# Kernel optimization log

Hardware: AMD Instinct MI355X
Metric: run time of the kernel (lower is better)

## Reference

```python
import jax, jax.numpy as jnp
import numpy as np

NUM_BLOCK = 8
CHANNELS = 256
SCALE = 0.02


def setup_inputs() -> dict:
    key = jax.random.key(0)
    k1, k2, k3, k4, k5, k6 = jax.random.split(key, 6)
    real = jax.random.normal(k1, (4, 4096, NUM_BLOCK, CHANNELS), dtype=jnp.float32)
    imag = jax.random.normal(k2, (4, 4096, NUM_BLOCK, CHANNELS), dtype=jnp.float32)
    w_r = jax.random.normal(k3, (NUM_BLOCK, CHANNELS, CHANNELS), dtype=jnp.float32) * SCALE
    w_i = jax.random.normal(k4, (NUM_BLOCK, CHANNELS, CHANNELS), dtype=jnp.float32) * SCALE
    b_r = jax.random.normal(k5, (NUM_BLOCK, CHANNELS), dtype=jnp.float32) * SCALE
    b_i = jax.random.normal(k6, (NUM_BLOCK, CHANNELS), dtype=jnp.float32) * SCALE
    return {"real": real, "imag": imag, "w_r": w_r, "w_i": w_i, "b_r": b_r, "b_i": b_i}


def _mm(x, w):
    # x: [..., b, d], w: [b, d, k] -> [..., b, k]
    return jnp.einsum('...bd,bdk->...bk', x, w)


def reference(real, imag, w_r, w_i, b_r, b_i):
    out_r = _mm(real, w_r) - _mm(imag, w_i) + b_r
    out_i = _mm(real, w_i) + _mm(imag, w_r) + b_i
    return (out_r, out_i)
```

## Files before the change

kernel.cpp:

```cpp
#include <hip/hip_runtime.h>
#include <hip/hip_bf16.h>

#define NB 8
#define CH 256
#define MTOT 16384
#define ROWSTRIDE 2048
#define BM 128
#define KSTEPS 8
#define LDSPITCH 40
#define ABUF 10240
#define AIOFF 5120
#define OFFI 33554432l

typedef __attribute__((ext_vector_type(8))) short bf16x8;
typedef __attribute__((ext_vector_type(4))) float f32x4;

__device__ inline short f2bf(float f) {
    union { float f; unsigned u; } x{f};
    unsigned r = x.u + 0x7fff + ((x.u >> 16) & 1);
    return (short)(r >> 16);
}

__global__ void prep_w(const float* __restrict__ wr, const float* __restrict__ wi,
                       unsigned short* __restrict__ wT) {
    int blk = blockIdx.x;
    int mat = blk >> 8;
    int idx = blk & 255;
    int nc = idx & 3, kc = (idx >> 2) & 7, b = idx >> 5;
    const float* w = mat ? wi : wr;
    __shared__ float tile[32][65];
    int t = threadIdx.x;
    int dd = t >> 3;
    int nn = (t & 7) * 8;
    const float* src = w + (((size_t)b * 256 + kc * 32 + dd) * 256 + nc * 64 + nn);
#pragma unroll
    for (int j = 0; j < 8; ++j) tile[dd][nn + j] = src[j];
    __syncthreads();
    int n = t >> 2;
    int ds = (t & 3) * 8;
    bf16x8 p;
#pragma unroll
    for (int j = 0; j < 8; ++j) p[j] = f2bf(tile[ds + j][n]);
    unsigned short* dst = wT + (size_t)mat * 524288 + b * 65536 + kc * 8192
                             + (nc * 64 + n) * 32 + ds;
    *(bf16x8*)dst = p;
}

__launch_bounds__(512, 2)
__global__ void cgemm(const float* __restrict__ Ar, const float* __restrict__ Ai,
                      const unsigned short* __restrict__ wT,
                      const float* __restrict__ br, const float* __restrict__ bi,
                      float* __restrict__ out) {
    int bid = blockIdx.x;
    int b  = bid & 7;
    int mt = bid >> 3;

    __shared__ unsigned short lds[2 * ABUF];

    int t = threadIdx.x;
    int lane = t & 63;
    int wv = t >> 6;
    int wr_ = wv >> 2;
    int wc_ = wv & 3;
    int lrow = lane & 15;
    int kseg = lane >> 4;

    int srow = t >> 2;
    int sseg = t & 3;
    const size_t a_base = (size_t)(mt * BM + srow) * ROWSTRIDE + b * CH + sseg * 8;

    const unsigned short* wbase = wT + (size_t)b * 65536
                                     + (wc_ * 64 + lrow) * 32 + kseg * 8;

    f32x4 accr[4][4] = {};
    f32x4 acci[4][4] = {};

    f32x4 rR0, rR1, rI0, rI1;
    bf16x8 rwr[2][4], rwi[2][4];

#define LOADA(K) { const float* p = Ar + a_base + (size_t)(K) * 32;              \
                   rR0 = *(const f32x4*)p;  rR1 = *(const f32x4*)(p + 4);        \
                   const float* q = Ai + a_base + (size_t)(K) * 32;              \
                   rI0 = *(const f32x4*)q;  rI1 = *(const f32x4*)(q + 4); }
#define LOADW(SEL, K) {                                                          \
    const unsigned short* p = wbase + (size_t)(K) * 8192;                        \
    rwr[SEL][0] = *(const bf16x8*)p;                                             \
    rwr[SEL][1] = *(const bf16x8*)(p + 512);                                     \
    rwr[SEL][2] = *(const bf16x8*)(p + 1024);                                    \
    rwr[SEL][3] = *(const bf16x8*)(p + 1536);                                    \
    rwi[SEL][0] = *(const bf16x8*)(p + 524288);                                  \
    rwi[SEL][1] = *(const bf16x8*)(p + 524800);                                  \
    rwi[SEL][2] = *(const bf16x8*)(p + 525312);                                  \
    rwi[SEL][3] = *(const bf16x8*)(p + 525824); }
#define STAGEA(BUF) {                                                            \
    bf16x8 pr, pi;                                                               \
    _Pragma("unroll")                                                            \
    for (int j = 0; j < 4; ++j) { pr[j] = f2bf(rR0[j]); pr[j + 4] = f2bf(rR1[j]);\
                                  pi[j] = f2bf(rI0[j]); pi[j + 4] = f2bf(rI1[j]);}\
    int d0 = (BUF) * ABUF + srow * LDSPITCH + sseg * 8;                          \
    *(bf16x8*)&lds[d0]         = pr;                                             \
    *(bf16x8*)&lds[d0 + AIOFF] = pi; }

    LOADA(0);
    LOADW(0, 0);
    STAGEA(0);

#pragma unroll
    for (int kk = 0; kk < KSTEPS; ++kk) {
        __syncthreads();
        if (kk + 1 < KSTEPS) {
            LOADA(kk + 1);
            LOADW((kk + 1) & 1, kk + 1);
        }
        int ab = (kk & 1) * ABUF;
#pragma unroll
        for (int mf = 0; mf < 4; ++mf) {
            int off = ab + (wr_ * 64 + mf * 16 + lrow) * LDSPITCH + kseg * 8;
            bf16x8 ar = *(const bf16x8*)&lds[off];
            bf16x8 ai = *(const bf16x8*)&lds[off + AIOFF];
            bf16x8 ain = ai ^ (short)0x8000;
#pragma unroll
            for (int nf = 0; nf < 4; ++nf) {
                accr[mf][nf] = __builtin_amdgcn_mfma_f32_16x16x32_bf16(ar,  rwr[kk & 1][nf], accr[mf][nf], 0, 0, 0);
                accr[mf][nf] = __builtin_amdgcn_mfma_f32_16x16x32_bf16(ain, rwi[kk & 1][nf], accr[mf][nf], 0, 0, 0);
                acci[mf][nf] = __builtin_amdgcn_mfma_f32_16x16x32_bf16(ar,  rwi[kk & 1][nf], acci[mf][nf], 0, 0, 0);
                acci[mf][nf] = __builtin_amdgcn_mfma_f32_16x16x32_bf16(ai,  rwr[kk & 1][nf], acci[mf][nf], 0, 0, 0);
            }
        }
        if (kk + 1 < KSTEPS) STAGEA((kk + 1) & 1);
    }

    int colb = wc_ * 64 + lrow;
    int rbase = mt * BM + wr_ * 64 + (lane >> 4) * 4;
#pragma unroll
    for (int nf = 0; nf < 4; ++nf) {
        int col = colb + nf * 16;
        float brv = br[b * CH + col];
        float biv = bi[b * CH + col];
#pragma unroll
        for (int mf = 0; mf < 4; ++mf) {
            size_t ro = (size_t)(rbase + mf * 16) * ROWSTRIDE + b * CH + col;
#pragma unroll
            for (int j = 0; j < 4; ++j) {
                out[ro + (size_t)j * ROWSTRIDE]        = accr[mf][nf][j] + brv;
                out[OFFI + ro + (size_t)j * ROWSTRIDE] = acci[mf][nf][j] + biv;
            }
        }
    }
#undef LOADA
#undef LOADW
#undef STAGEA
}

extern "C" void kernel_launch(void* const* d_in, const int* in_sizes, int n_in,
                              void* d_out, int out_size, void* d_ws, size_t ws_size,
                              hipStream_t stream) {
    const float* real = (const float*)d_in[0];
    const float* imag = (const float*)d_in[1];
    const float* w_r  = (const float*)d_in[2];
    const float* w_i  = (const float*)d_in[3];
    const float* b_r  = (const float*)d_in[4];
    const float* b_i  = (const float*)d_in[5];
    float* out = (float*)d_out;
    unsigned short* wT = (unsigned short*)d_ws;

    prep_w<<<512, 256, 0, stream>>>(w_r, w_i, wT);
    cgemm<<<(MTOT / BM) * NB, 512, 0, stream>>>(real, imag, wT, b_r, b_i, out);
}
```

Before: 463.2 us.

## Halve row tile to 64 with 256-thread blocks and explicit ping-pong weight registers

Shrinks the M tile from 128 to 64 rows and the block from 512 to 256 threads (4 waves, each covering all 64 rows), which doubles the grid. The k-loop is unrolled by two with named register sets for double-buffered weights instead of an indexed array, so no dynamic register indexing is possible. The aim is more blocks per CU and better latency hiding. In exchange, each weight fragment fetched from global memory is reused across half as many rows, so weight traffic doubles.

```diff
diff --git a/kernel.cpp b/kernel.cpp
--- a/kernel.cpp
+++ b/kernel.cpp
@@ -5,11 +5,11 @@
 #define CH 256
 #define MTOT 16384
 #define ROWSTRIDE 2048
-#define BM 128
+#define BM 64
 #define KSTEPS 8
 #define LDSPITCH 40
-#define ABUF 10240
-#define AIOFF 5120
+#define ABUF 5120
+#define AIOFF 2560
 #define OFFI 33554432l
 
 typedef __attribute__((ext_vector_type(8))) short bf16x8;
@@ -46,7 +46,7 @@
     *(bf16x8*)dst = p;
 }
 
-__launch_bounds__(512, 2)
+__launch_bounds__(256, 2)
 __global__ void cgemm(const float* __restrict__ Ar, const float* __restrict__ Ai,
                       const unsigned short* __restrict__ wT,
                       const float* __restrict__ br, const float* __restrict__ bi,
@@ -59,9 +59,7 @@
 
     int t = threadIdx.x;
     int lane = t & 63;
-    int wv = t >> 6;
-    int wr_ = wv >> 2;
-    int wc_ = wv & 3;
+    int wc_ = t >> 6;
     int lrow = lane & 15;
     int kseg = lane >> 4;
 
@@ -76,22 +74,22 @@
     f32x4 acci[4][4] = {};
 
     f32x4 rR0, rR1, rI0, rI1;
-    bf16x8 rwr[2][4], rwi[2][4];
+    bf16x8 wrA[4], wiA[4], wrB[4], wiB[4];
 
 #define LOADA(K) { const float* p = Ar + a_base + (size_t)(K) * 32;              \
                    rR0 = *(const f32x4*)p;  rR1 = *(const f32x4*)(p + 4);        \
                    const float* q = Ai + a_base + (size_t)(K) * 32;              \
                    rI0 = *(const f32x4*)q;  rI1 = *(const f32x4*)(q + 4); }
-#define LOADW(SEL, K) {                                                          \
+#define LOADW(WR, WI, K) {                                                       \
     const unsigned short* p = wbase + (size_t)(K) * 8192;                        \
-    rwr[SEL][0] = *(const bf16x8*)p;                                             \
-    rwr[SEL][1] = *(const bf16x8*)(p + 512);                                     \
-    rwr[SEL][2] = *(const bf16x8*)(p + 1024);                                    \
-    rwr[SEL][3] = *(const bf16x8*)(p + 1536);                                    \
-    rwi[SEL][0] = *(const bf16x8*)(p + 524288);                                  \
-    rwi[SEL][1] = *(const bf16x8*)(p + 524800);                                  \
-    rwi[SEL][2] = *(const bf16x8*)(p + 525312);                                  \
-    rwi[SEL][3] = *(const bf16x8*)(p + 525824); }
+    WR[0] = *(const bf16x8*)p;                                                   \
+    WR[1] = *(const bf16x8*)(p + 512);                                           \
+    WR[2] = *(const bf16x8*)(p + 1024);                                          \
+    WR[3] = *(const bf16x8*)(p + 1536);                                          \
+    WI[0] = *(const bf16x8*)(p + 524288);                                        \
+    WI[1] = *(const bf16x8*)(p + 524800);                                        \
+    WI[2] = *(const bf16x8*)(p + 525312);                                        \
+    WI[3] = *(const bf16x8*)(p + 525824); }
 #define STAGEA(BUF) {                                                            \
     bf16x8 pr, pi;                                                               \
     _Pragma("unroll")                                                            \
@@ -100,38 +98,41 @@
     int d0 = (BUF) * ABUF + srow * LDSPITCH + sseg * 8;                          \
     *(bf16x8*)&lds[d0]         = pr;                                             \
     *(bf16x8*)&lds[d0 + AIOFF] = pi; }
+#define MFMAS(AB, WR, WI) {                                                      \
+    _Pragma("unroll")                                                            \
+    for (int mf = 0; mf < 4; ++mf) {                                             \
+        int off = (AB) + (mf * 16 + lrow) * LDSPITCH + kseg * 8;                 \
+        bf16x8 ar = *(const bf16x8*)&lds[off];                                   \
+        bf16x8 ai = *(const bf16x8*)&lds[off + AIOFF];                           \
+        bf16x8 ain = ai ^ (short)0x8000;                                         \
+        _Pragma("unroll")                                                        \
+        for (int nf = 0; nf < 4; ++nf) {                                         \
+            accr[mf][nf] = __builtin_amdgcn_mfma_f32_16x16x32_bf16(ar,  WR[nf], accr[mf][nf], 0, 0, 0); \
+            accr[mf][nf] = __builtin_amdgcn_mfma_f32_16x16x32_bf16(ain, WI[nf], accr[mf][nf], 0, 0, 0); \
+            acci[mf][nf] = __builtin_amdgcn_mfma_f32_16x16x32_bf16(ar,  WI[nf], acci[mf][nf], 0, 0, 0); \
+            acci[mf][nf] = __builtin_amdgcn_mfma_f32_16x16x32_bf16(ai,  WR[nf], acci[mf][nf], 0, 0, 0); \
+        }                                                                        \
+    } }
 
     LOADA(0);
-    LOADW(0, 0);
+    LOADW(wrA, wiA, 0);
     STAGEA(0);
 
 #pragma unroll
-    for (int kk = 0; kk < KSTEPS; ++kk) {
+    for (int kt = 0; kt < 4; ++kt) {
         __syncthreads();
-        if (kk + 1 < KSTEPS) {
-            LOADA(kk + 1);
-            LOADW((kk + 1) & 1, kk + 1);
-        }
-        int ab = (kk & 1) * ABUF;
-#pragma unroll
-        for (int mf = 0; mf < 4; ++mf) {
-            int off = ab + (wr_ * 64 + mf * 16 + lrow) * LDSPITCH + kseg * 8;
-            bf16x8 ar = *(const bf16x8*)&lds[off];
-            bf16x8 ai = *(const bf16x8*)&lds[off + AIOFF];
-            bf16x8 ain = ai ^ (short)0x8000;
-#pragma unroll
-            for (int nf = 0; nf < 4; ++nf) {
-                accr[mf][nf] = __builtin_amdgcn_mfma_f32_16x16x32_bf16(ar,  rwr[kk & 1][nf], accr[mf][nf], 0, 0, 0);
-                accr[mf][nf] = __builtin_amdgcn_mfma_f32_16x16x32_bf16(ain, rwi[kk & 1][nf], accr[mf][nf], 0, 0, 0);
-                acci[mf][nf] = __builtin_amdgcn_mfma_f32_16x16x32_bf16(ar,  rwi[kk & 1][nf], acci[mf][nf], 0, 0, 0);
-                acci[mf][nf] = __builtin_amdgcn_mfma_f32_16x16x32_bf16(ai,  rwr[kk & 1][nf], acci[mf][nf], 0, 0, 0);
-            }
-        }
-        if (kk + 1 < KSTEPS) STAGEA((kk + 1) & 1);
+        LOADA(2 * kt + 1);
+        LOADW(wrB, wiB, 2 * kt + 1);
+        MFMAS(0, wrA, wiA);
+        STAGEA(1);
+        __syncthreads();
+        if (kt < 3) { LOADA(2 * kt + 2); LOADW(wrA, wiA, 2 * kt + 2); }
+        MFMAS(ABUF, wrB, wiB);
+        if (kt < 3) STAGEA(0);
     }
 
     int colb = wc_ * 64 + lrow;
-    int rbase = mt * BM + wr_ * 64 + (lane >> 4) * 4;
+    int rbase = mt * BM + (lane >> 4) * 4;
 #pragma unroll
     for (int nf = 0; nf < 4; ++nf) {
         int col = colb + nf * 16;
@@ -150,6 +151,7 @@
 #undef LOADA
 #undef LOADW
 #undef STAGEA
+#undef MFMAS
 }
 
 extern "C" void kernel_launch(void* const* d_in, const int* in_sizes, int n_in,
@@ -165,5 +167,5 @@
     unsigned short* wT = (unsigned short*)d_ws;
 
     prep_w<<<512, 256, 0, stream>>>(w_r, w_i, wT);
-    cgemm<<<(MTOT / BM) * NB, 512, 0, stream>>>(real, imag, wT, b_r, b_i, out);
+    cgemm<<<(MTOT / BM) * NB, 256, 0, stream>>>(real, imag, wT, b_r, b_i, out);
 }
```

Result: slower. 484.1 us (+4.5%).
